# Performance work log

Hardware: AMD Instinct MI355X
Metric: run time of the kernel (lower is better)

Reference implementation:

```python
import jax, jax.numpy as jnp
import numpy as np
import math

B, N, C = 8, 2048, 512

def setup_inputs() -> dict:
    key = jax.random.key(0)
    ks = jax.random.split(key, 7)
    s = 1.0 / math.sqrt(C)
    return {
        "feature": jax.random.normal(ks[0], (B, N, C), dtype=jnp.float32),
        "wq": jax.random.uniform(ks[1], (C, C), jnp.float32, -s, s),
        "bq": jax.random.uniform(ks[2], (C,), jnp.float32, -s, s),
        "wk": jax.random.uniform(ks[3], (C, C), jnp.float32, -s, s),
        "bk": jax.random.uniform(ks[4], (C,), jnp.float32, -s, s),
        "wv": jax.random.uniform(ks[5], (C, C), jnp.float32, -s, s),
        "bv": jax.random.uniform(ks[6], (C,), jnp.float32, -s, s),
    }

def reference(feature, wq, bq, wk, bk, wv, bv):
    # torch nn.Linear: x @ W.T + b
    q = jnp.einsum('bnc,dc->bnd', feature, wq) + bq
    k = jnp.einsum('bnc,dc->bnd', feature, wk) + bk
    v = jnp.einsum('bnc,dc->bnd', feature, wv) + bv
    scores = jnp.einsum('bnd,bmd->bnm', q, k)          # [B, N, N]
    attn = jax.nn.softmax(scores, axis=2) / math.sqrt(C)  # post-softmax scale (as in source)
    v_star = jnp.einsum('bnm,bmd->bnd', attn, v)
    return feature + v_star
```

## Files before the change

kernel.cpp:

```cpp
#include <hip/hip_runtime.h>
#include <cstdint>
#include <cstddef>


typedef __bf16 bf16x8 __attribute__((ext_vector_type(8)));
typedef float f32x4 __attribute__((ext_vector_type(4)));
typedef short short4v __attribute__((ext_vector_type(4)));
typedef short short8v __attribute__((ext_vector_type(8)));

__device__ __forceinline__ float b2f(short s) {
  union { float f; unsigned u; } u; u.u = ((unsigned)(unsigned short)s) << 16; return u.f;
}
__device__ __forceinline__ short f2b(float f) {
  union { float f; unsigned u; } u; u.f = f;
  unsigned r = (u.u + 0x7fffu + ((u.u >> 16) & 1u)) >> 16;
  return (short)r;
}

#define GLDS(gptr, lptr) \
  __builtin_amdgcn_global_load_lds( \
      (const __attribute__((address_space(1))) unsigned int*)(const void*)(gptr), \
      (__attribute__((address_space(3))) unsigned int*)(void*)(lptr), 16, 0, 0)

__global__ __launch_bounds__(256) void prep(const float* __restrict__ f,
                                            const float* __restrict__ w0,
                                            const float* __restrict__ w1,
                                            const float* __restrict__ w2,
                                            const float* __restrict__ b0,
                                            const float* __restrict__ b1,
                                            const float* __restrict__ b2,
                                            short* __restrict__ Xb, short* __restrict__ Wb,
                                            float* __restrict__ biasP, float* __restrict__ l) {
  const int bid = blockIdx.x;
  const int t = threadIdx.x;
  if (bid < 8192) {
    int i = bid * 256 + t;
    float4 v = ((const float4*)f)[i];
    short4v o = { f2b(v.x), f2b(v.y), f2b(v.z), f2b(v.w) };
    *(short4v*)(Xb + (size_t)i * 4) = o;
  } else if (bid < 8960) {
    int i = (bid - 8192) * 256 + t;
    const float* src = (i < 65536) ? w0 : (i < 131072) ? w1 : w2;
    float4 v = ((const float4*)src)[i & 65535];
    short4v o = { f2b(v.x), f2b(v.y), f2b(v.z), f2b(v.w) };
    *(short4v*)(Wb + (size_t)i * 4) = o;
  } else {
    int i = (bid - 8960) * 256 + t;
    float4 z = { 0.f, 0.f, 0.f, 0.f };
    ((float4*)l)[i * 2] = z;
    ((float4*)l)[i * 2 + 1] = z;
    if (i < 1536) {
      const float* s = (i < 512) ? b0 : (i < 1024) ? b1 : b2;
      biasP[i] = s[i & 511];
    }
  }
}

__global__ __launch_bounds__(256) void gemm_qkv(const short* __restrict__ X,
                                                const short* __restrict__ Wall,
                                                const float* __restrict__ biasP,
                                                short* __restrict__ Out) {
  __shared__ __align__(16) short Xs[128 * 32];
  __shared__ __align__(16) short Ws[128 * 32];
  const int z = blockIdx.z;
  const short* Wm = Wall + (size_t)z * 262144;
  const int m0 = blockIdx.y * 128, n0 = blockIdx.x * 128;
  const int t = threadIdx.x;
  const int lane = t & 63, w = t >> 6;
  const int wn = (w & 1) * 64, wm = (w >> 1) * 64;
  const int fr = lane & 15, fk = (lane >> 4) * 8;

  f32x4 acc[4][4] = {};
  const int c0 = t, c1 = t + 256;
  const int r0 = c0 >> 2, k80 = (c0 & 3) * 8;
  const int r1 = c1 >> 2, k81 = (c1 & 3) * 8;

  for (int k0 = 0; k0 < 512; k0 += 32) {
    __syncthreads();
    GLDS(X + (size_t)(m0 + r0) * 512 + k0 + k80, Xs + c0 * 8);
    GLDS(X + (size_t)(m0 + r1) * 512 + k0 + k81, Xs + c1 * 8);
    GLDS(Wm + (size_t)(n0 + r0) * 512 + k0 + k80, Ws + c0 * 8);
    GLDS(Wm + (size_t)(n0 + r1) * 512 + k0 + k81, Ws + c1 * 8);
    __syncthreads();
    bf16x8 wf[4], xf[4];
#pragma unroll
    for (int i = 0; i < 4; ++i) wf[i] = *(const bf16x8*)(Ws + (wn + i * 16 + fr) * 32 + fk);
#pragma unroll
    for (int j = 0; j < 4; ++j) xf[j] = *(const bf16x8*)(Xs + (wm + j * 16 + fr) * 32 + fk);
#pragma unroll
    for (int i = 0; i < 4; ++i)
#pragma unroll
      for (int j = 0; j < 4; ++j)
        acc[i][j] = __builtin_amdgcn_mfma_f32_16x16x32_bf16(wf[i], xf[j], acc[i][j], 0, 0, 0);
  }

  const int rq = (lane >> 4) * 4;
#pragma unroll
  for (int i = 0; i < 4; ++i) {
    int nb = n0 + wn + i * 16 + rq;
    float4 bs = *(const float4*)(biasP + z * 512 + nb);
#pragma unroll
    for (int j = 0; j < 4; ++j) {
      int m = m0 + wm + j * 16 + fr;
      short4v o = { f2b(acc[i][j][0] + bs.x), f2b(acc[i][j][1] + bs.y),
                    f2b(acc[i][j][2] + bs.z), f2b(acc[i][j][3] + bs.w) };
      *(short4v*)(Out + (size_t)z * 8388608 + (size_t)m * 512 + nb) = o;
    }
  }
}

__global__ __launch_bounds__(256) void gemm_qk(const short* __restrict__ Q,
                                               const short* __restrict__ Kb,
                                               short* __restrict__ P,
                                               float* __restrict__ l) {
  __shared__ __align__(16) short Qs[128 * 32];
  __shared__ __align__(16) short Ks[128 * 32];
  const int z = blockIdx.z;
  const short* A = Q + (size_t)z * 2048 * 512;
  const short* Bm = Kb + (size_t)z * 2048 * 512;
  const int m0 = blockIdx.y * 128, n0 = blockIdx.x * 128;
  const int t = threadIdx.x;
  const int lane = t & 63, w = t >> 6;
  const int wn = (w & 1) * 64, wm = (w >> 1) * 64;
  const int fr = lane & 15, fk = (lane >> 4) * 8;

  f32x4 acc[4][4] = {};
  const int c0 = t, c1 = t + 256;
  const int r0 = c0 >> 2, k80 = (c0 & 3) * 8;
  const int r1 = c1 >> 2, k81 = (c1 & 3) * 8;

  for (int k0 = 0; k0 < 512; k0 += 32) {
    __syncthreads();
    GLDS(A + (size_t)(m0 + r0) * 512 + k0 + k80, Qs + c0 * 8);
    GLDS(A + (size_t)(m0 + r1) * 512 + k0 + k81, Qs + c1 * 8);
    GLDS(Bm + (size_t)(n0 + r0) * 512 + k0 + k80, Ks + c0 * 8);
    GLDS(Bm + (size_t)(n0 + r1) * 512 + k0 + k81, Ks + c1 * 8);
    __syncthreads();
    bf16x8 kf[4], qf[4];
#pragma unroll
    for (int i = 0; i < 4; ++i) kf[i] = *(const bf16x8*)(Ks + (wn + i * 16 + fr) * 32 + fk);
#pragma unroll
    for (int j = 0; j < 4; ++j) qf[j] = *(const bf16x8*)(Qs + (wm + j * 16 + fr) * 32 + fk);
#pragma unroll
    for (int i = 0; i < 4; ++i)
#pragma unroll
      for (int j = 0; j < 4; ++j)
        acc[i][j] = __builtin_amdgcn_mfma_f32_16x16x32_bf16(kf[i], qf[j], acc[i][j], 0, 0, 0);
  }

  const int rq = (lane >> 4) * 4;
  float rs[4] = { 0.f, 0.f, 0.f, 0.f };
#pragma unroll
  for (int i = 0; i < 4; ++i) {
    int nb = n0 + wn + i * 16 + rq;
#pragma unroll
    for (int j = 0; j < 4; ++j) {
      int m = m0 + wm + j * 16 + fr;
      short4v o;
      float part = 0.f;
#pragma unroll
      for (int r = 0; r < 4; ++r) {
        float e = exp2f(acc[i][j][r] * 1.4426950408889634f);
        short eb = f2b(e);
        o[r] = eb;
        part += b2f(eb);
      }
      *(short4v*)(P + (size_t)z * 4194304 + (size_t)m * 2048 + nb) = o;
      rs[j] += part;
    }
  }
#pragma unroll
  for (int j = 0; j < 4; ++j) {
    rs[j] += __shfl_xor(rs[j], 16);
    rs[j] += __shfl_xor(rs[j], 32);
  }
  if (lane < 16) {
#pragma unroll
    for (int j = 0; j < 4; ++j)
      atomicAdd(&l[z * 2048 + m0 + wm + j * 16 + fr], rs[j]);
  }
}

__global__ __launch_bounds__(256) void gemm_pv(const short* __restrict__ Pm,
                                               const short* __restrict__ Vt,
                                               const float* __restrict__ l,
                                               const float* __restrict__ resid,
                                               float* __restrict__ out, float scale) {
  __shared__ __align__(16) short Ps[64 * 32];
  __shared__ __align__(16) short Vs[128 * 32];
  const int z = blockIdx.z;
  const short* A = Pm + (size_t)z * 4194304;
  const short* Bm = Vt + (size_t)z * 1048576;
  const int m0 = blockIdx.y * 64, n0 = blockIdx.x * 128;
  const int t = threadIdx.x;
  const int lane = t & 63, w = t >> 6;
  const int wn = (w & 1) * 64, wm = (w >> 1) * 32;
  const int fr = lane & 15, fk = (lane >> 4) * 8;

  f32x4 acc[4][2] = {};
  const int ra = t >> 2, k8a = (t & 3) * 8;
  const int c0 = t, c1 = t + 256;
  const int r0 = c0 >> 2, k80 = (c0 & 3) * 8;
  const int r1 = c1 >> 2, k81 = (c1 & 3) * 8;

  for (int k0 = 0; k0 < 2048; k0 += 32) {
    __syncthreads();
    GLDS(A + (size_t)(m0 + ra) * 2048 + k0 + k8a, Ps + t * 8);
    GLDS(Bm + (size_t)(n0 + r0) * 2048 + k0 + k80, Vs + c0 * 8);
    GLDS(Bm + (size_t)(n0 + r1) * 2048 + k0 + k81, Vs + c1 * 8);
    __syncthreads();
    bf16x8 vf[4], pf[2];
#pragma unroll
    for (int i = 0; i < 4; ++i) vf[i] = *(const bf16x8*)(Vs + (wn + i * 16 + fr) * 32 + fk);
#pragma unroll
    for (int j = 0; j < 2; ++j) pf[j] = *(const bf16x8*)(Ps + (wm + j * 16 + fr) * 32 + fk);
#pragma unroll
    for (int i = 0; i < 4; ++i)
#pragma unroll
      for (int j = 0; j < 2; ++j)
        acc[i][j] = __builtin_amdgcn_mfma_f32_16x16x32_bf16(vf[i], pf[j], acc[i][j], 0, 0, 0);
  }

  const int rq = (lane >> 4) * 4;
#pragma unroll
  for (int j = 0; j < 2; ++j) {
    int m = m0 + wm + j * 16 + fr;
    float linv = scale / l[z * 2048 + m];
#pragma unroll
    for (int i = 0; i < 4; ++i) {
      int nb = n0 + wn + i * 16 + rq;
      size_t idx = (size_t)z * 1048576 + (size_t)m * 512 + nb;
      float4 rv = *(const float4*)(resid + idx);
      float4 o = { rv.x + acc[i][j][0] * linv, rv.y + acc[i][j][1] * linv,
                   rv.z + acc[i][j][2] * linv, rv.w + acc[i][j][3] * linv };
      *(float4*)(out + idx) = o;
    }
  }
}

__global__ __launch_bounds__(256) void transpose64(const short* __restrict__ V,
                                                   short* __restrict__ Vt) {
  __shared__ short tile[64][72];
  const int b = blockIdx.z;
  const int d0 = blockIdx.x * 64, n0 = blockIdx.y * 64;
  const int t = threadIdx.x;
#pragma unroll
  for (int h = 0; h < 2; ++h) {
    int c = t + h * 256;
    int r = c >> 3, cj = (c & 7) * 8;
    short8v val = *(const short8v*)(V + ((size_t)(b * 2048 + n0 + r)) * 512 + d0 + cj);
#pragma unroll
    for (int j = 0; j < 8; ++j) tile[r][cj + j] = val[j];
  }
  __syncthreads();
#pragma unroll
  for (int h = 0; h < 2; ++h) {
    int c = t + h * 256;
    int dr = c >> 3, nj = (c & 7) * 8;
    short8v o;
#pragma unroll
    for (int j = 0; j < 8; ++j) o[j] = tile[nj + j][dr];
    *(short8v*)(Vt + ((size_t)b * 512 + d0 + dr) * 2048 + n0 + nj) = o;
  }
}

extern "C" void kernel_launch(void* const* d_in, const int* in_sizes, int n_in,
                              void* d_out, int out_size, void* d_ws, size_t ws_size,
                              hipStream_t stream) {
  const float* feature = (const float*)d_in[0];
  const float* wq = (const float*)d_in[1];
  const float* bq = (const float*)d_in[2];
  const float* wk = (const float*)d_in[3];
  const float* bk = (const float*)d_in[4];
  const float* wv = (const float*)d_in[5];
  const float* bv = (const float*)d_in[6];
  float* out = (float*)d_out;

  const size_t MN = (size_t)16384 * 512;
  short* Xb = (short*)d_ws;
  short* Wb = Xb + MN;
  short* Q = Wb + 786432;
  short* K = Q + MN;
  short* V = K + MN;
  short* Vt = V + MN;
  short* P = Vt + MN;
  float* biasP = (float*)(P + (size_t)8 * 2048 * 2048);
  float* l = biasP + 1536;

  prep<<<8968, 256, 0, stream>>>(feature, wq, wk, wv, bq, bk, bv, Xb, Wb, biasP, l);

  gemm_qkv<<<dim3(4, 128, 3), 256, 0, stream>>>(Xb, Wb, biasP, Q);
  transpose64<<<dim3(8, 32, 8), 256, 0, stream>>>(V, Vt);
  gemm_qk<<<dim3(16, 16, 8), 256, 0, stream>>>(Q, K, P, l);

  const float iscl = 0.044194173824159216f;
  gemm_pv<<<dim3(4, 32, 8), 256, 0, stream>>>(P, Vt, l, feature, out, iscl);
}
```

Before: 270.6 us.

## Fuse QK^T, exp and PV into a single flash-style attention kernel

Replaces the separate QK^T kernel (which wrote the full bf16 P matrix and atomically accumulated row sums) and the PV kernel with one fused kernel. Each block keeps a 64-row Q tile in LDS, streams K and V tiles, computes unnormalized exp scores into LDS and accumulates the output directly. The aim is to drop the large P round-trip through global memory, the global atomics and a launch. In exchange the grid is only 256 blocks of 512 threads, the loops are not double-buffered and there are many barriers, so occupancy and latency hiding may suffer.

```diff
diff --git a/kernel.cpp b/kernel.cpp
--- a/kernel.cpp
+++ b/kernel.cpp
@@ -30,7 +30,7 @@
                                             const float* __restrict__ b1,
                                             const float* __restrict__ b2,
                                             short* __restrict__ Xb, short* __restrict__ Wb,
-                                            float* __restrict__ biasP, float* __restrict__ l) {
+                                            float* __restrict__ biasP) {
   const int bid = blockIdx.x;
   const int t = threadIdx.x;
   if (bid < 8192) {
@@ -46,9 +46,6 @@
     *(short4v*)(Wb + (size_t)i * 4) = o;
   } else {
     int i = (bid - 8960) * 256 + t;
-    float4 z = { 0.f, 0.f, 0.f, 0.f };
-    ((float4*)l)[i * 2] = z;
-    ((float4*)l)[i * 2 + 1] = z;
     if (i < 1536) {
       const float* s = (i < 512) ? b0 : (i < 1024) ? b1 : b2;
       biasP[i] = s[i & 511];
@@ -109,135 +106,6 @@
   }
 }
 
-__global__ __launch_bounds__(256) void gemm_qk(const short* __restrict__ Q,
-                                               const short* __restrict__ Kb,
-                                               short* __restrict__ P,
-                                               float* __restrict__ l) {
-  __shared__ __align__(16) short Qs[128 * 32];
-  __shared__ __align__(16) short Ks[128 * 32];
-  const int z = blockIdx.z;
-  const short* A = Q + (size_t)z * 2048 * 512;
-  const short* Bm = Kb + (size_t)z * 2048 * 512;
-  const int m0 = blockIdx.y * 128, n0 = blockIdx.x * 128;
-  const int t = threadIdx.x;
-  const int lane = t & 63, w = t >> 6;
-  const int wn = (w & 1) * 64, wm = (w >> 1) * 64;
-  const int fr = lane & 15, fk = (lane >> 4) * 8;
-
-  f32x4 acc[4][4] = {};
-  const int c0 = t, c1 = t + 256;
-  const int r0 = c0 >> 2, k80 = (c0 & 3) * 8;
-  const int r1 = c1 >> 2, k81 = (c1 & 3) * 8;
-
-  for (int k0 = 0; k0 < 512; k0 += 32) {
-    __syncthreads();
-    GLDS(A + (size_t)(m0 + r0) * 512 + k0 + k80, Qs + c0 * 8);
-    GLDS(A + (size_t)(m0 + r1) * 512 + k0 + k81, Qs + c1 * 8);
-    GLDS(Bm + (size_t)(n0 + r0) * 512 + k0 + k80, Ks + c0 * 8);
-    GLDS(Bm + (size_t)(n0 + r1) * 512 + k0 + k81, Ks + c1 * 8);
-    __syncthreads();
-    bf16x8 kf[4], qf[4];
-#pragma unroll
-    for (int i = 0; i < 4; ++i) kf[i] = *(const bf16x8*)(Ks + (wn + i * 16 + fr) * 32 + fk);
-#pragma unroll
-    for (int j = 0; j < 4; ++j) qf[j] = *(const bf16x8*)(Qs + (wm + j * 16 + fr) * 32 + fk);
-#pragma unroll
-    for (int i = 0; i < 4; ++i)
-#pragma unroll
-      for (int j = 0; j < 4; ++j)
-        acc[i][j] = __builtin_amdgcn_mfma_f32_16x16x32_bf16(kf[i], qf[j], acc[i][j], 0, 0, 0);
-  }
-
-  const int rq = (lane >> 4) * 4;
-  float rs[4] = { 0.f, 0.f, 0.f, 0.f };
-#pragma unroll
-  for (int i = 0; i < 4; ++i) {
-    int nb = n0 + wn + i * 16 + rq;
-#pragma unroll
-    for (int j = 0; j < 4; ++j) {
-      int m = m0 + wm + j * 16 + fr;
-      short4v o;
-      float part = 0.f;
-#pragma unroll
-      for (int r = 0; r < 4; ++r) {
-        float e = exp2f(acc[i][j][r] * 1.4426950408889634f);
-        short eb = f2b(e);
-        o[r] = eb;
-        part += b2f(eb);
-      }
-      *(short4v*)(P + (size_t)z * 4194304 + (size_t)m * 2048 + nb) = o;
-      rs[j] += part;
-    }
-  }
-#pragma unroll
-  for (int j = 0; j < 4; ++j) {
-    rs[j] += __shfl_xor(rs[j], 16);
-    rs[j] += __shfl_xor(rs[j], 32);
-  }
-  if (lane < 16) {
-#pragma unroll
-    for (int j = 0; j < 4; ++j)
-      atomicAdd(&l[z * 2048 + m0 + wm + j * 16 + fr], rs[j]);
-  }
-}
-
-__global__ __launch_bounds__(256) void gemm_pv(const short* __restrict__ Pm,
-                                               const short* __restrict__ Vt,
-                                               const float* __restrict__ l,
-                                               const float* __restrict__ resid,
-                                               float* __restrict__ out, float scale) {
-  __shared__ __align__(16) short Ps[64 * 32];
-  __shared__ __align__(16) short Vs[128 * 32];
-  const int z = blockIdx.z;
-  const short* A = Pm + (size_t)z * 4194304;
-  const short* Bm = Vt + (size_t)z * 1048576;
-  const int m0 = blockIdx.y * 64, n0 = blockIdx.x * 128;
-  const int t = threadIdx.x;
-  const int lane = t & 63, w = t >> 6;
-  const int wn = (w & 1) * 64, wm = (w >> 1) * 32;
-  const int fr = lane & 15, fk = (lane >> 4) * 8;
-
-  f32x4 acc[4][2] = {};
-  const int ra = t >> 2, k8a = (t & 3) * 8;
-  const int c0 = t, c1 = t + 256;
-  const int r0 = c0 >> 2, k80 = (c0 & 3) * 8;
-  const int r1 = c1 >> 2, k81 = (c1 & 3) * 8;
-
-  for (int k0 = 0; k0 < 2048; k0 += 32) {
-    __syncthreads();
-    GLDS(A + (size_t)(m0 + ra) * 2048 + k0 + k8a, Ps + t * 8);
-    GLDS(Bm + (size_t)(n0 + r0) * 2048 + k0 + k80, Vs + c0 * 8);
-    GLDS(Bm + (size_t)(n0 + r1) * 2048 + k0 + k81, Vs + c1 * 8);
-    __syncthreads();
-    bf16x8 vf[4], pf[2];
-#pragma unroll
-    for (int i = 0; i < 4; ++i) vf[i] = *(const bf16x8*)(Vs + (wn + i * 16 + fr) * 32 + fk);
-#pragma unroll
-    for (int j = 0; j < 2; ++j) pf[j] = *(const bf16x8*)(Ps + (wm + j * 16 + fr) * 32 + fk);
-#pragma unroll
-    for (int i = 0; i < 4; ++i)
-#pragma unroll
-      for (int j = 0; j < 2; ++j)
-        acc[i][j] = __builtin_amdgcn_mfma_f32_16x16x32_bf16(vf[i], pf[j], acc[i][j], 0, 0, 0);
-  }
-
-  const int rq = (lane >> 4) * 4;
-#pragma unroll
-  for (int j = 0; j < 2; ++j) {
-    int m = m0 + wm + j * 16 + fr;
-    float linv = scale / l[z * 2048 + m];
-#pragma unroll
-    for (int i = 0; i < 4; ++i) {
-      int nb = n0 + wn + i * 16 + rq;
-      size_t idx = (size_t)z * 1048576 + (size_t)m * 512 + nb;
-      float4 rv = *(const float4*)(resid + idx);
-      float4 o = { rv.x + acc[i][j][0] * linv, rv.y + acc[i][j][1] * linv,
-                   rv.z + acc[i][j][2] * linv, rv.w + acc[i][j][3] * linv };
-      *(float4*)(out + idx) = o;
-    }
-  }
-}
-
 __global__ __launch_bounds__(256) void transpose64(const short* __restrict__ V,
                                                    short* __restrict__ Vt) {
   __shared__ short tile[64][72];
@@ -261,6 +129,119 @@
 #pragma unroll
     for (int j = 0; j < 8; ++j) o[j] = tile[nj + j][dr];
     *(short8v*)(Vt + ((size_t)b * 512 + d0 + dr) * 2048 + n0 + nj) = o;
+  }
+}
+
+__global__ __launch_bounds__(512, 2) void fused_attn(const short* __restrict__ Qg,
+                                                     const short* __restrict__ Kg,
+                                                     const short* __restrict__ Vt,
+                                                     const float* __restrict__ resid,
+                                                     float* __restrict__ out, float scale) {
+  __shared__ __align__(16) short Qs[64 * 520];
+  __shared__ __align__(16) short Ks[2 * 128 * 32];
+  __shared__ __align__(16) short Vs[512 * 32];
+  __shared__ __align__(16) short Ps[64 * 136];
+  __shared__ float Lsum[64];
+
+  const int z = blockIdx.y;
+  const int m0 = blockIdx.x * 64;
+  const int t = threadIdx.x;
+  const int lane = t & 63, w = t >> 6;
+  const int fr = lane & 15, l4 = lane >> 4;
+  const int wk2 = (w & 1) * 64, wq = (w >> 1) * 16;
+  const int wd = (w >> 1) * 128, wq2 = (w & 1) * 32;
+
+  const short* Qrow = Qg + ((size_t)z * 2048 + m0) * 512;
+  const short* Krow = Kg + (size_t)z * 2048 * 512;
+  const short* Vrow = Vt + (size_t)z * 512 * 2048;
+
+  if (t < 64) Lsum[t] = 0.f;
+
+  {
+    const int row = t >> 3, col = (t & 7) * 64;
+#pragma unroll
+    for (int u = 0; u < 8; ++u) {
+      short8v v = *(const short8v*)(Qrow + (size_t)row * 512 + col + u * 8);
+      *(short8v*)(Qs + row * 520 + col + u * 8) = v;
+    }
+  }
+
+  f32x4 acc_o[8][2] = {};
+  float l_acc = 0.f;
+
+  for (int kt = 0; kt < 16; ++kt) {
+    const int kb = kt * 128;
+    f32x4 acc_s[4] = {};
+
+    for (int c = 0; c < 8; ++c) {
+      __syncthreads();
+#pragma unroll
+      for (int u = 0; u < 2; ++u) {
+        int cc = t + u * 512;
+        int cb = cc >> 9, rr = (cc >> 2) & 127, k8 = (cc & 3) * 8;
+        GLDS(Krow + (size_t)(kb + rr) * 512 + c * 64 + cb * 32 + k8, Ks + cc * 8);
+      }
+      __syncthreads();
+#pragma unroll
+      for (int h = 0; h < 2; ++h) {
+        bf16x8 qf = *(const bf16x8*)(Qs + (wq + fr) * 520 + c * 64 + h * 32 + l4 * 8);
+#pragma unroll
+        for (int i = 0; i < 4; ++i) {
+          bf16x8 kf = *(const bf16x8*)(Ks + h * 4096 + (wk2 + 16 * i + fr) * 32 + l4 * 8);
+          acc_s[i] = __builtin_amdgcn_mfma_f32_16x16x32_bf16(kf, qf, acc_s[i], 0, 0, 0);
+        }
+      }
+    }
+
+#pragma unroll
+    for (int i = 0; i < 4; ++i) {
+      short4v p4;
+#pragma unroll
+      for (int r = 0; r < 4; ++r) {
+        float e = exp2f(acc_s[i][r] * 1.4426950408889634f);
+        short eb = f2b(e);
+        p4[r] = eb;
+        l_acc += b2f(eb);
+      }
+      *(short4v*)(Ps + (wq + fr) * 136 + wk2 + 16 * i + l4 * 4) = p4;
+    }
+
+    for (int kc = 0; kc < 4; ++kc) {
+      __syncthreads();
+#pragma unroll
+      for (int u = 0; u < 4; ++u) {
+        int cc = t + u * 512;
+        int dd = cc >> 2, k8 = (cc & 3) * 8;
+        GLDS(Vrow + (size_t)dd * 2048 + kb + kc * 32 + k8, Vs + cc * 8);
+      }
+      __syncthreads();
+      bf16x8 pf0 = *(const bf16x8*)(Ps + (wq2 + fr) * 136 + kc * 32 + l4 * 8);
+      bf16x8 pf1 = *(const bf16x8*)(Ps + (wq2 + 16 + fr) * 136 + kc * 32 + l4 * 8);
+#pragma unroll
+      for (int i = 0; i < 8; ++i) {
+        bf16x8 vf = *(const bf16x8*)(Vs + (wd + 16 * i + fr) * 32 + l4 * 8);
+        acc_o[i][0] = __builtin_amdgcn_mfma_f32_16x16x32_bf16(vf, pf0, acc_o[i][0], 0, 0, 0);
+        acc_o[i][1] = __builtin_amdgcn_mfma_f32_16x16x32_bf16(vf, pf1, acc_o[i][1], 0, 0, 0);
+      }
+    }
+  }
+
+  atomicAdd(&Lsum[wq + fr], l_acc);
+  __syncthreads();
+
+#pragma unroll
+  for (int j = 0; j < 2; ++j) {
+    int q2 = wq2 + 16 * j + fr;
+    float linv = scale / Lsum[q2];
+#pragma unroll
+    for (int i = 0; i < 8; ++i) {
+      int d0 = wd + 16 * i + l4 * 4;
+      size_t idx = ((size_t)z * 2048 + m0 + q2) * 512 + d0;
+      float4 rv = *(const float4*)(resid + idx);
+      float4 o = { rv.x + acc_o[i][j][0] * linv, rv.y + acc_o[i][j][1] * linv,
+                   rv.z + acc_o[i][j][2] * linv, rv.w + acc_o[i][j][3] * linv };
+      *(float4*)(out + idx) = o;
+    }
   }
 }
 
@@ -283,16 +264,12 @@
   short* K = Q + MN;
   short* V = K + MN;
   short* Vt = V + MN;
-  short* P = Vt + MN;
-  float* biasP = (float*)(P + (size_t)8 * 2048 * 2048);
-  float* l = biasP + 1536;
-
-  prep<<<8968, 256, 0, stream>>>(feature, wq, wk, wv, bq, bk, bv, Xb, Wb, biasP, l);
-
+  float* biasP = (float*)(Vt + MN);
+
+  prep<<<8966, 256, 0, stream>>>(feature, wq, wk, wv, bq, bk, bv, Xb, Wb, biasP);
   gemm_qkv<<<dim3(4, 128, 3), 256, 0, stream>>>(Xb, Wb, biasP, Q);
   transpose64<<<dim3(8, 32, 8), 256, 0, stream>>>(V, Vt);
-  gemm_qk<<<dim3(16, 16, 8), 256, 0, stream>>>(Q, K, P, l);
 
   const float iscl = 0.044194173824159216f;
-  gemm_pv<<<dim3(4, 32, 8), 256, 0, stream>>>(P, Vt, l, feature, out, iscl);
-}
+  fused_attn<<<dim3(32, 8), 512, 0, stream>>>(Q, K, Vt, feature, out, iscl);
+}
```

Result: slower. 315.8 us (+16.7%).
